# Performance work log

Hardware: AMD Instinct MI355X
Metric: run time of the kernel (lower is better)

## Reference

```python
import jax, jax.numpy as jnp
import numpy as np

B, Q, E, NH, L, P = 8, 1024, 256, 8, 4, 4
DH = E // NH
SHAPES = np.array([[128, 128], [64, 64], [32, 32], [16, 16]], dtype=np.int64)
STARTS = np.concatenate([[0], np.cumsum(SHAPES.prod(1))[:-1]]).astype(np.int64)
S_TOTAL = int(SHAPES.prod(1).sum())
EPS = 1e-5


def setup_inputs() -> dict:
    key = jax.random.key(0)
    ks = iter(jax.random.split(key, 40))
    def rn(shp, s=0.02):
        return jax.random.normal(next(ks), shp, jnp.float32) * s
    return {
        "tgt": rn((B, Q, E), 1.0),
        "query_pos": rn((B, Q, E), 1.0),
        "reference_points": jax.random.uniform(next(ks), (B, Q, L, 2), jnp.float32),
        "src": rn((B, S_TOTAL, E), 1.0),
        "spatial_shapes": jnp.asarray(SHAPES),
        "level_start_index": jnp.asarray(STARTS),
        "in_proj_w": rn((3 * E, E)), "in_proj_b": jnp.zeros((3 * E,), jnp.float32),
        "out_proj_w": rn((E, E)), "out_proj_b": jnp.zeros((E,), jnp.float32),
        "norm1_g": jnp.ones((E,), jnp.float32), "norm1_b": jnp.zeros((E,), jnp.float32),
        "off_w": rn((NH * L * P * 2, E)), "off_b": rn((NH * L * P * 2,), 0.5),
        "aw_w": rn((NH * L * P, E)), "aw_b": jnp.zeros((NH * L * P,), jnp.float32),
        "vp_w": rn((E, E)), "vp_b": jnp.zeros((E,), jnp.float32),
        "op_w": rn((E, E)), "op_b": jnp.zeros((E,), jnp.float32),
        "norm2_g": jnp.ones((E,), jnp.float32), "norm2_b": jnp.zeros((E,), jnp.float32),
        "w1": rn((4 * E, E)), "b1": jnp.zeros((4 * E,), jnp.float32),
        "w2": rn((E, 4 * E)), "b2": jnp.zeros((E,), jnp.float32),
        "norm3_g": jnp.ones((E,), jnp.float32), "norm3_b": jnp.zeros((E,), jnp.float32),
    }


def _ln(x, g, b):
    mu = x.mean(-1, keepdims=True)
    var = ((x - mu) ** 2).mean(-1, keepdims=True)
    return (x - mu) * jax.lax.rsqrt(var + EPS) * g + b


def _bilinear(v, loc, Hl, Wl):
    # v: [B,NH,S_l,DH], loc in [0,1]: [B,NH,Q,P,2] -> [B,NH,Q,P,DH]
    # matches torch grid_sample(align_corners=False, padding='zeros')
    x = loc[..., 0] * Wl - 0.5
    y = loc[..., 1] * Hl - 0.5
    x0 = jnp.floor(x)
    y0 = jnp.floor(y)
    wx = (x - x0)[..., None]
    wy = (y - y0)[..., None]
    def g(yi, xi):
        valid = ((xi >= 0) & (xi <= Wl - 1) & (yi >= 0) & (yi <= Hl - 1)).astype(v.dtype)
        idx = (jnp.clip(yi, 0, Hl - 1) * Wl + jnp.clip(xi, 0, Wl - 1)).astype(jnp.int32)
        out = jnp.take_along_axis(v, idx.reshape(B, NH, Q * P, 1), axis=2)
        return out.reshape(B, NH, Q, P, DH) * valid[..., None]
    v00 = g(y0, x0); v01 = g(y0, x0 + 1.0)
    v10 = g(y0 + 1.0, x0); v11 = g(y0 + 1.0, x0 + 1.0)
    return (v00 * (1 - wy) * (1 - wx) + v01 * (1 - wy) * wx
            + v10 * wy * (1 - wx) + v11 * wy * wx)


def _forward(tgt, query_pos, reference_points, src,
             in_proj_w, in_proj_b, out_proj_w, out_proj_b, norm1_g, norm1_b,
             off_w, off_b, aw_w, aw_b, vp_w, vp_b, op_w, op_b,
             norm2_g, norm2_b, w1, b1, w2, b2, norm3_g, norm3_b,
             spatial_shapes, level_start_index):
    shp = np.asarray(spatial_shapes)
    starts = np.asarray(level_start_index)
    # ---- self-attention (q = k = tgt + pos, v = tgt) ----
    qk = tgt + query_pos
    wq, wk, wv = jnp.split(in_proj_w, 3, axis=0)
    bq, bk, bv = jnp.split(in_proj_b, 3, axis=0)
    q = (qk @ wq.T + bq).reshape(B, Q, NH, DH)
    k = (qk @ wk.T + bk).reshape(B, Q, NH, DH)
    v = (tgt @ wv.T + bv).reshape(B, Q, NH, DH)
    scores = jnp.einsum("bqhd,bkhd->bhqk", q, k) / jnp.sqrt(jnp.float32(DH))
    attn = jax.nn.softmax(scores, axis=-1)
    ctx = jnp.einsum("bhqk,bkhd->bqhd", attn, v).reshape(B, Q, E)
    tgt = _ln(tgt + (ctx @ out_proj_w.T + out_proj_b), norm1_g, norm1_b)
    # ---- MSDA cross-attention ----
    query = tgt + query_pos
    value = (src @ vp_w.T + vp_b).reshape(B, S_TOTAL, NH, DH).transpose(0, 2, 1, 3)  # [B,NH,S,DH]
    off = (query @ off_w.T + off_b).reshape(B, Q, NH, L, P, 2)
    aw = jax.nn.softmax((query @ aw_w.T + aw_b).reshape(B, Q, NH, L * P), -1)
    aw = aw.reshape(B, Q, NH, L, P)
    normalizer = jnp.asarray(shp[:, ::-1].copy(), jnp.float32)  # [L,2] = (W,H)
    loc = reference_points[:, :, None, :, None, :] + off / normalizer[None, None, None, :, None, :]
    loc = jnp.transpose(loc, (0, 2, 1, 3, 4, 5))  # [B,NH,Q,L,P,2]
    awt = jnp.transpose(aw, (0, 2, 1, 3, 4))      # [B,NH,Q,L,P]
    out = jnp.zeros((B, NH, Q, DH), jnp.float32)
    for l in range(L):
        Hl, Wl = int(shp[l, 0]), int(shp[l, 1])
        s0 = int(starts[l])
        vl = value[:, :, s0:s0 + Hl * Wl]
        samp = _bilinear(vl, loc[:, :, :, l], Hl, Wl)         # [B,NH,Q,P,DH]
        out = out + (samp * awt[:, :, :, l, :, None]).sum(3)
    ca = out.transpose(0, 2, 1, 3).reshape(B, Q, E) @ op_w.T + op_b
    tgt = _ln(tgt + ca, norm2_g, norm2_b)
    # ---- FFN ----
    h = jax.nn.relu(tgt @ w1.T + b1) @ w2.T + b2
    return _ln(tgt + h, norm3_g, norm3_b)


def reference(tgt, query_pos, reference_points, src, spatial_shapes, level_start_index,
              in_proj_w, in_proj_b, out_proj_w, out_proj_b, norm1_g, norm1_b,
              off_w, off_b, aw_w, aw_b, vp_w, vp_b, op_w, op_b,
              norm2_g, norm2_b, w1, b1, w2, b2, norm3_g, norm3_b):
    return _forward(tgt, query_pos, reference_points, src,
                    in_proj_w, in_proj_b, out_proj_w, out_proj_b, norm1_g, norm1_b,
                    off_w, off_b, aw_w, aw_b, vp_w, vp_b, op_w, op_b,
                    norm2_g, norm2_b, w1, b1, w2, b2, norm3_g, norm3_b,
                    spatial_shapes, level_start_index)
```

## Files before the change

### kernel.cpp

```cpp
#include <hip/hip_runtime.h>
#include <hip/hip_bf16.h>
#include <math.h>

typedef __hip_bfloat16 bf16;
typedef unsigned short ushort_t;

#define BQ 8
#define QLEN 1024
#define EMB 256
#define NHD 8
#define NLVL 4
#define NPT 4
#define DHD 32
#define STOT 21760

typedef short s8v __attribute__((ext_vector_type(8)));
typedef float f4v __attribute__((ext_vector_type(4)));

__device__ __forceinline__ float b2f(bf16 x) { return __bfloat162float(x); }

__device__ __forceinline__ float ldin(const void* p, int bf, size_t i) {
    return bf ? __bfloat162float(((const bf16*)p)[i]) : ((const float*)p)[i];
}

__device__ __forceinline__ float bfraw(unsigned u) {
    union { unsigned i; float f; } c; c.i = u << 16; return c.f;
}

__device__ __forceinline__ unsigned short f2us(float x) {
    bf16 h = __float2bfloat16(x);
    unsigned short u;
    __builtin_memcpy(&u, &h, 2);
    return u;
}

__device__ __forceinline__ void ld4(const void* p, int bf, size_t i, float* o) {
    if (bf) {
        const uint2 u = *(const uint2*)((const ushort_t*)p + i);
        o[0] = bfraw(u.x & 0xffffu); o[1] = bfraw(u.x >> 16);
        o[2] = bfraw(u.y & 0xffffu); o[3] = bfraw(u.y >> 16);
    } else {
        const float4 f = *(const float4*)((const float*)p + i);
        o[0] = f.x; o[1] = f.y; o[2] = f.z; o[3] = f.w;
    }
}

typedef const __attribute__((address_space(1))) unsigned int* gas1_u32;
typedef __attribute__((address_space(3))) unsigned int* las3_u32;
__device__ __forceinline__ void gload_lds16(const void* g, void* l) {
    __builtin_amdgcn_global_load_lds((gas1_u32)g, (las3_u32)l, 16, 0, 0);
}

__global__ void detect_dtype(const unsigned* __restrict__ n1g, int* __restrict__ flag) {
    if (threadIdx.x == 0) flag[0] = (n1g[0] == 0x3F800000u) ? 0 : 1;
}

template <int BN, int KT, int WAVES, bool ARAW, bool RELU, typename CT>
__global__ __launch_bounds__(WAVES * 64) void gemm_wlds(
        const void* __restrict__ A,
        const void* __restrict__ W, int w0,
        const void* __restrict__ bias, int b0,
        CT* __restrict__ C,
        int M, int N,
        const int* __restrict__ dflag) {
    constexpr int T = WAVES * 64;
    constexpr int GPR = KT / 8;
    constexpr int WSLOTS = BN * GPR;
    constexpr int NJ = BN / 16;
    constexpr int KC = KT / 256;
    constexpr int CW = BN < 128 ? BN : 128;
    constexpr int NCH = BN / CW;
    constexpr int JC = CW / 16;
    constexpr int ST_US = (sizeof(CT) == 2) ? (CW + 8) : 2 * (CW + 12);
    constexpr int EPI_US = WAVES * 16 * ST_US;
    constexpr int SMEM_US = (BN * KT) > EPI_US ? (BN * KT) : EPI_US;

    __shared__ __align__(16) ushort_t smem[SMEM_US];

    const int bfm = *dflag;
    const int tid = threadIdx.x;
    const int lane = tid & 63;
    const int wv = tid >> 6;
    const int l15 = lane & 15, lhi = lane >> 4;
    const int n0 = blockIdx.x * BN;
    const int mg = blockIdx.y * (16 * WAVES) + wv * 16;

#pragma unroll
    for (int i = 0; i < WSLOTS / T; ++i) {
        const int s0 = (wv << 6) + T * i;
        const int s = s0 + lane;
        const int n = s / GPR;
        const int gl = s & (GPR - 1);
        const int gg = (gl + GPR - (n & (GPR - 1))) & (GPR - 1);
        const size_t woff = (size_t)(w0 + n0 + n) * KT + gg * 8;
        if (bfm) {
            gload_lds16((const ushort_t*)W + woff, smem + (size_t)s0 * 8);
        } else {
            const float* wf = (const float*)W + woff;
            const float4 f0 = *(const float4*)wf;
            const float4 f1 = *(const float4*)(wf + 4);
            ushort_t t[8] = {f2us(f0.x), f2us(f0.y), f2us(f0.z), f2us(f0.w),
                             f2us(f1.x), f2us(f1.y), f2us(f1.z), f2us(f1.w)};
            *(uint4*)(smem + (size_t)s * 8) = *(uint4*)t;
        }
    }

    auto ldA = [&](int kc, s8v* af) {
#pragma unroll
        for (int kk = 0; kk < 8; ++kk) {
            const size_t ao = (size_t)(mg + l15) * KT + kc * 256 + kk * 32 + lhi * 8;
            if (!ARAW || bfm) {
                af[kk] = *(const s8v*)((const ushort_t*)A + ao);
            } else {
                const float* ap = (const float*)A + ao;
                const float4 f0 = *(const float4*)ap;
                const float4 f1 = *(const float4*)(ap + 4);
                ushort_t t[8] = {f2us(f0.x), f2us(f0.y), f2us(f0.z), f2us(f0.w),
                                 f2us(f1.x), f2us(f1.y), f2us(f1.z), f2us(f1.w)};
                af[kk] = *(const s8v*)t;
            }
        }
    };

    f4v acc[NJ] = {};
    s8v afA[8], afB[8];
    ldA(0, afA);
    __syncthreads();

#pragma unroll
    for (int kc = 0; kc < KC; ++kc) {
        s8v* af = (kc & 1) ? afB : afA;
        s8v* afn = (kc & 1) ? afA : afB;
        if (kc + 1 < KC) ldA(kc + 1, afn);
#pragma unroll
        for (int j = 0; j < NJ; ++j) {
            const int n = j * 16 + l15;
#pragma unroll
            for (int kk = 0; kk < 8; ++kk) {
                const int gg = kc * 32 + kk * 4 + lhi;
                const int gl = (gg + n) & (GPR - 1);
                const s8v b = *(const s8v*)(smem + (size_t)n * KT + gl * 8);
                acc[j] = __builtin_amdgcn_mfma_f32_16x16x32_bf16(af[kk], b, acc[j], 0, 0, 0);
            }
        }
    }
    __syncthreads();

    if constexpr (sizeof(CT) == 2) {
        ushort_t* eb = smem + wv * 16 * ST_US;
#pragma unroll
        for (int c = 0; c < NCH; ++c) {
#pragma unroll
            for (int jj = 0; jj < JC; ++jj) {
                const int j = c * JC + jj;
                const float bv = ldin(bias, bfm, b0 + n0 + j * 16 + l15);
#pragma unroll
                for (int p = 0; p < 4; ++p) {
                    float v = acc[j][p] + bv;
                    if (RELU) v = fmaxf(v, 0.f);
                    eb[(lhi * 4 + p) * ST_US + jj * 16 + l15] = f2us(v);
                }
            }
            asm volatile("s_waitcnt lgkmcnt(0)" ::: "memory");
            __builtin_amdgcn_sched_barrier(0);
            constexpr int GPRow = CW / 8;
            constexpr int RPP = 64 / GPRow;
#pragma unroll
            for (int pass = 0; pass < 16 / RPP; ++pass) {
                const int row = pass * RPP + lane / GPRow;
                const int g = lane % GPRow;
                const uint4 u = *(const uint4*)(eb + row * ST_US + g * 8);
                *(uint4*)((ushort_t*)C + (size_t)(mg + row) * N + n0 + c * CW + g * 8) = u;
            }
            asm volatile("s_waitcnt lgkmcnt(0)" ::: "memory");
            __builtin_amdgcn_sched_barrier(0);
        }
    } else {
        constexpr int ST_F = CW + 12;
        float* ef = (float*)(smem) + wv * 16 * ST_F;
#pragma unroll
        for (int c = 0; c < NCH; ++c) {
#pragma unroll
            for (int jj = 0; jj < JC; ++jj) {
                const int j = c * JC + jj;
                const float bv = ldin(bias, bfm, b0 + n0 + j * 16 + l15);
#pragma unroll
                for (int p = 0; p < 4; ++p) {
                    float v = acc[j][p] + bv;
                    if (RELU) v = fmaxf(v, 0.f);
                    ef[(lhi * 4 + p) * ST_F + jj * 16 + l15] = v;
                }
            }
            asm volatile("s_waitcnt lgkmcnt(0)" ::: "memory");
            __builtin_amdgcn_sched_barrier(0);
            constexpr int GPRow = CW / 4;
            constexpr int RPP = 64 / GPRow;
#pragma unroll
            for (int pass = 0; pass < 16 / RPP; ++pass) {
                const int row = pass * RPP + lane / GPRow;
                const int g = lane % GPRow;
                const float4 u = *(const float4*)(ef + row * ST_F + g * 4);
                *(float4*)((float*)C + (size_t)(mg + row) * N + n0 + c * CW + g * 4) = u;
            }
            asm volatile("s_waitcnt lgkmcnt(0)" ::: "memory");
            __builtin_amdgcn_sched_barrier(0);
        }
    }
}

__global__ void ew_add_bf(const void* __restrict__ a, const void* __restrict__ b,
                          ushort_t* __restrict__ c, int n4, const int* __restrict__ dflag) {
    const int bfm = *dflag;
    const int i = blockIdx.x * 256 + threadIdx.x;
    if (i < n4) {
        float ta[4], tb[4];
        ld4(a, bfm, (size_t)i * 4, ta);
        ld4(b, bfm, (size_t)i * 4, tb);
        uint2 u;
        u.x = (unsigned)f2us(ta[0] + tb[0]) | ((unsigned)f2us(ta[1] + tb[1]) << 16);
        u.y = (unsigned)f2us(ta[2] + tb[2]) | ((unsigned)f2us(ta[3] + tb[3]) << 16);
        *(uint2*)(c + (size_t)i * 4) = u;
    }
}

__global__ __launch_bounds__(256) void attn_mfma(const ushort_t* __restrict__ qkbuf,
                                                 const ushort_t* __restrict__ v,
                                                 ushort_t* __restrict__ ctx) {
    __shared__ ushort_t Ks[64][40];
    __shared__ ushort_t Vt[32][72];
    __shared__ ushort_t Ps[4][16][72];
    const int bh = blockIdx.y;
    const int b = bh >> 3, h = bh & 7;
    const int qt = blockIdx.x;
    const int tid = threadIdx.x;
    const int lane = tid & 63;
    const int wv = tid >> 6;
    const int l15 = lane & 15, quad = lane >> 4;
    const float scale = 0.17677669529663689f;

    const int qbase = (qt << 6) + (wv << 4);
    const s8v qfrag = *(const s8v*)(qkbuf +
        ((size_t)(b * QLEN + qbase + l15)) * 512 + h * DHD + quad * 8);

    const int sk = tid >> 2;
    const int sd = (tid & 3) << 3;

    float m_run[4] = {-1e30f, -1e30f, -1e30f, -1e30f};
    float l_run[4] = {};
    f4v o[2] = {};

    for (int kt = 0; kt < 16; ++kt) {
        __syncthreads();
        const size_t krow = (size_t)(b * QLEN + (kt << 6) + sk);
        *(uint4*)&Ks[sk][sd] = *(const uint4*)(qkbuf + krow * 512 + 256 + h * DHD + sd);
        const uint4 uv = *(const uint4*)(v + krow * 256 + h * DHD + sd);
        ushort_t vt[8];
        *(uint4*)vt = uv;
#pragma unroll
        for (int j = 0; j < 8; ++j) Vt[sd + j][sk] = vt[j];
        __syncthreads();

        f4v s4[4];
#pragma unroll
        for (int kb = 0; kb < 4; ++kb) {
            const s8v kfr = *(const s8v*)&Ks[(kb << 4) + l15][quad * 8];
            s4[kb] = __builtin_amdgcn_mfma_f32_16x16x32_bf16(qfrag, kfr, f4v{}, 0, 0, 0);
        }

        float sc[4][4];
#pragma unroll
        for (int kb = 0; kb < 4; ++kb)
#pragma unroll
            for (int p = 0; p < 4; ++p) sc[kb][p] = s4[kb][p] * scale;
        float mp[4];
#pragma unroll
        for (int p = 0; p < 4; ++p)
            mp[p] = fmaxf(fmaxf(sc[0][p], sc[1][p]), fmaxf(sc[2][p], sc[3][p]));
#pragma unroll
        for (int p = 0; p < 4; ++p) {
            mp[p] = fmaxf(mp[p], __shfl_xor(mp[p], 1, 64));
            mp[p] = fmaxf(mp[p], __shfl_xor(mp[p], 2, 64));
            mp[p] = fmaxf(mp[p], __shfl_xor(mp[p], 4, 64));
            mp[p] = fmaxf(mp[p], __shfl_xor(mp[p], 8, 64));
        }
        float al[4], ls[4] = {};
#pragma unroll
        for (int p = 0; p < 4; ++p) {
            const float mn = fmaxf(m_run[p], mp[p]);
            al[p] = __expf(m_run[p] - mn);
            m_run[p] = mn;
        }
        float pe[4][4];
#pragma unroll
        for (int kb = 0; kb < 4; ++kb)
#pragma unroll
            for (int p = 0; p < 4; ++p) {
                const float e = __expf(sc[kb][p] - m_run[p]);
                pe[kb][p] = e;
                ls[p] += e;
            }
#pragma unroll
        for (int p = 0; p < 4; ++p) {
            ls[p] += __shfl_xor(ls[p], 1, 64);
            ls[p] += __shfl_xor(ls[p], 2, 64);
            ls[p] += __shfl_xor(ls[p], 4, 64);
            ls[p] += __shfl_xor(ls[p], 8, 64);
            l_run[p] = l_run[p] * al[p] + ls[p];
        }
#pragma unroll
        for (int nb = 0; nb < 2; ++nb)
#pragma unroll
            for (int p = 0; p < 4; ++p) o[nb][p] *= al[p];

#pragma unroll
        for (int kb = 0; kb < 4; ++kb)
#pragma unroll
            for (int p = 0; p < 4; ++p)
                Ps[wv][(quad << 2) + p][(kb << 4) + l15] = f2us(pe[kb][p]);

#pragma unroll
        for (int kk = 0; kk < 2; ++kk) {
            const s8v afr = *(const s8v*)&Ps[wv][l15][kk * 32 + quad * 8];
#pragma unroll
            for (int nb = 0; nb < 2; ++nb) {
                const s8v bfr = *(const s8v*)&Vt[nb * 16 + l15][kk * 32 + quad * 8];
                o[nb] = __builtin_amdgcn_mfma_f32_16x16x32_bf16(afr, bfr, o[nb], 0, 0, 0);
            }
        }
    }

#pragma unroll
    for (int p = 0; p < 4; ++p) {
        const float inv = 1.f / l_run[p];
        const size_t row = (size_t)(b * QLEN + qbase + (quad << 2) + p) * EMB + h * DHD;
#pragma unroll
        for (int nb = 0; nb < 2; ++nb)
            ctx[row + nb * 16 + l15] = f2us(o[nb][p] * inv);
    }
}

__global__ __launch_bounds__(256) void ln_kernel(const void* __restrict__ xb,
                                                 const float* __restrict__ xf1,
                                                 const float* __restrict__ xf2,
                                                 const void* __restrict__ g,
                                                 const void* __restrict__ bta,
                                                 float* __restrict__ out_f,
                                                 ushort_t* __restrict__ out_b,
                                                 void* __restrict__ out_d,
                                                 const void* __restrict__ qp,
                                                 ushort_t* __restrict__ out_q,
                                                 const int* __restrict__ dflag) {
    const int bf = *dflag;
    const int row = blockIdx.x * 4 + (threadIdx.x >> 6);
    const int lane = threadIdx.x & 63;
    const size_t base = (size_t)row * EMB + lane * 4;

    float x[4] = {0.f, 0.f, 0.f, 0.f};
    if (xb) {
        float t[4]; ld4(xb, bf, base, t);
#pragma unroll
        for (int j = 0; j < 4; ++j) x[j] += t[j];
    }
    if (xf1) {
        const float4 f = *(const float4*)(xf1 + base);
        x[0] += f.x; x[1] += f.y; x[2] += f.z; x[3] += f.w;
    }
    if (xf2) {
        const float4 f = *(const float4*)(xf2 + base);
        x[0] += f.x; x[1] += f.y; x[2] += f.z; x[3] += f.w;
    }
    float s = x[0] + x[1] + x[2] + x[3];
#pragma unroll
    for (int o = 1; o < 64; o <<= 1) s += __shfl_xor(s, o, 64);
    const float mu = s * (1.f / EMB);
    float dx[4], vs = 0.f;
#pragma unroll
    for (int j = 0; j < 4; ++j) { dx[j] = x[j] - mu; vs += dx[j] * dx[j]; }
#pragma unroll
    for (int o = 1; o < 64; o <<= 1) vs += __shfl_xor(vs, o, 64);
    const float inv = rsqrtf(vs * (1.f / EMB) + 1e-5f);

    float gv[4], bv[4];
    ld4(g, bf, (size_t)lane * 4, gv);
    ld4(bta, bf, (size_t)lane * 4, bv);
    float y[4];
#pragma unroll
    for (int j = 0; j < 4; ++j) y[j] = dx[j] * inv * gv[j] + bv[j];

    if (out_f) *(float4*)(out_f + base) = float4{y[0], y[1], y[2], y[3]};
    if (out_b) {
        uint2 u;
        u.x = (unsigned)f2us(y[0]) | ((unsigned)f2us(y[1]) << 16);
        u.y = (unsigned)f2us(y[2]) | ((unsigned)f2us(y[3]) << 16);
        *(uint2*)(out_b + base) = u;
    }
    if (out_d) {
        if (bf) {
            uint2 u;
            u.x = (unsigned)f2us(y[0]) | ((unsigned)f2us(y[1]) << 16);
            u.y = (unsigned)f2us(y[2]) | ((unsigned)f2us(y[3]) << 16);
            *(uint2*)((ushort_t*)out_d + base) = u;
        } else {
            *(float4*)((float*)out_d + base) = float4{y[0], y[1], y[2], y[3]};
        }
    }
    if (out_q) {
        float q[4]; ld4(qp, bf, base, q);
        uint2 u;
        u.x = (unsigned)f2us(y[0] + q[0]) | ((unsigned)f2us(y[1] + q[1]) << 16);
        u.y = (unsigned)f2us(y[2] + q[2]) | ((unsigned)f2us(y[3] + q[3]) << 16);
        *(uint2*)(out_q + base) = u;
    }
}

__global__ __launch_bounds__(64) void sample_kernel(const float* __restrict__ offb,
                                                    const float* __restrict__ awb,
                                                    const void* __restrict__ refp,
                                                    const ushort_t* __restrict__ value,
                                                    ushort_t* __restrict__ out,
                                                    const int* __restrict__ dflag) {
    const int bf = *dflag;
    const int bid = blockIdx.x;
    const int h = bid & 7;
    const int bq = bid >> 3;
    const int b = bq >> 10;
    const int lane = threadIdx.x;
    const int s_idx = lane >> 2;
    const int dg = lane & 3;
    const int l = s_idx >> 2;

    float logit = awb[(size_t)bq * 128 + h * 16 + s_idx];
    float m = logit;
#pragma unroll
    for (int o = 32; o > 0; o >>= 1) m = fmaxf(m, __shfl_xor(m, o, 64));
    float e = __expf(logit - m);
    float ssum = e;
#pragma unroll
    for (int o = 32; o > 0; o >>= 1) ssum += __shfl_xor(ssum, o, 64);
    const float paw = 4.f * e / ssum;

    const int Wi = 128 >> l;
    const float Wl = (float)Wi, Hl = (float)Wi;
    const int s0 = (l == 0) ? 0 : (l == 1) ? 16384 : (l == 2) ? 20480 : 21504;

    const float rx = ldin(refp, bf, ((size_t)bq * NLVL + l) * 2 + 0);
    const float ry = ldin(refp, bf, ((size_t)bq * NLVL + l) * 2 + 1);
    const float ox = offb[(size_t)bq * 256 + h * 32 + s_idx * 2 + 0];
    const float oy = offb[(size_t)bq * 256 + h * 32 + s_idx * 2 + 1];
    const float x = (rx + ox / Wl) * Wl - 0.5f;
    const float y = (ry + oy / Hl) * Hl - 0.5f;
    const float x0 = floorf(x), y0 = floorf(y);
    const float wx = x - x0, wy = y - y0;

    float acc[8] = {};
    const ushort_t* vbase = value + ((size_t)b * STOT) * EMB + h * DHD + dg * 8;

    auto corner = [&](float yi, float xi, float w) {
        const bool valid = (xi >= 0.f) && (xi <= Wl - 1.f) && (yi >= 0.f) && (yi <= Hl - 1.f);
        const float xc = fminf(fmaxf(xi, 0.f), Wl - 1.f);
        const float yc = fminf(fmaxf(yi, 0.f), Hl - 1.f);
        const int row = s0 + (int)yc * Wi + (int)xc;
        const uint4 u = *(const uint4*)(vbase + (size_t)row * EMB);
        const float wv = valid ? w : 0.f;
        const unsigned ua[4] = {u.x, u.y, u.z, u.w};
#pragma unroll
        for (int j = 0; j < 4; ++j) {
            acc[2 * j + 0] = fmaf(wv, bfraw(ua[j] & 0xffffu), acc[2 * j + 0]);
            acc[2 * j + 1] = fmaf(wv, bfraw(ua[j] >> 16), acc[2 * j + 1]);
        }
    };
    corner(y0, x0, (1.f - wy) * (1.f - wx));
    corner(y0, x0 + 1.f, (1.f - wy) * wx);
    corner(y0 + 1.f, x0, wy * (1.f - wx));
    corner(y0 + 1.f, x0 + 1.f, wy * wx);

#pragma unroll
    for (int j = 0; j < 8; ++j) {
        float vj = acc[j] * paw;
        vj += __shfl_xor(vj, 4, 64);
        vj += __shfl_xor(vj, 8, 64);
        vj += __shfl_xor(vj, 16, 64);
        vj += __shfl_xor(vj, 32, 64);
        acc[j] = vj;
    }
    if (s_idx == 0) {
        ushort_t t[8];
#pragma unroll
        for (int j = 0; j < 8; ++j) t[j] = f2us(acc[j]);
        *(uint4*)(out + (size_t)bq * EMB + h * DHD + dg * 8) = *(uint4*)t;
    }
}

extern "C" void kernel_launch(void* const* d_in, const int* in_sizes, int n_in,
                              void* d_out, int out_size, void* d_ws, size_t ws_size,
                              hipStream_t stream) {
    const void* tgt  = d_in[0];
    const void* qp   = d_in[1];
    const void* refp = d_in[2];
    const void* src  = d_in[3];
    const void* ipw  = d_in[6];
    const void* ipb  = d_in[7];
    const void* oprw = d_in[8];
    const void* oprb = d_in[9];
    const void* n1g  = d_in[10];
    const void* n1b  = d_in[11];
    const void* ofw  = d_in[12];
    const void* ofb  = d_in[13];
    const void* aww  = d_in[14];
    const void* awbv = d_in[15];
    const void* vpw  = d_in[16];
    const void* vpb  = d_in[17];
    const void* opw2 = d_in[18];
    const void* opb2 = d_in[19];
    const void* n2g  = d_in[20];
    const void* n2b  = d_in[21];
    const void* w1   = d_in[22];
    const void* b1   = d_in[23];
    const void* w2   = d_in[24];
    const void* b2   = d_in[25];
    const void* n3g  = d_in[26];
    const void* n3b  = d_in[27];

    const int M = BQ * QLEN;
    const int MS = BQ * STOT;

    char* ws = (char*)d_ws;
    int* dflag = (int*)ws;
    size_t o = 256;
    char* S1 = ws + o; o += (size_t)M * EMB * 2;
    char* S2 = ws + o; o += (size_t)M * 512 * 2;
    char* S3 = ws + o; o += (size_t)M * EMB * 2;
    char* S4 = ws + o; o += (size_t)M * EMB * 2;
    char* S5 = ws + o; o += (size_t)M * EMB * 4;
    char* S6 = ws + o; o += (size_t)M * EMB * 4;
    char* S7 = ws + o; o += (size_t)M * EMB * 4;
    char* S8 = ws + o;

    ushort_t* qk_bf    = (ushort_t*)S1;
    ushort_t* samp_bf  = (ushort_t*)S1;
    ushort_t* qkproj   = (ushort_t*)S2;
    float*    off_f    = (float*)S2;
    ushort_t* vproj    = (ushort_t*)S3;
    ushort_t* qry_bf   = (ushort_t*)S3;
    ushort_t* tgt2_bf  = (ushort_t*)S3;
    ushort_t* ctx_bf   = (ushort_t*)S4;
    float*    awl_f    = (float*)S4;
    float*    bufD     = (float*)S5;
    float*    tgt1_f   = (float*)S6;
    float*    tgt2_f   = (float*)S7;
    ushort_t* value_bf = (ushort_t*)S8;
    ushort_t* h1_bf    = (ushort_t*)S8;

    detect_dtype<<<1, 64, 0, stream>>>((const unsigned*)n1g, dflag);

    ew_add_bf<<<(M * EMB / 4) / 256, 256, 0, stream>>>(tgt, qp, qk_bf, M * EMB / 4, dflag);
    gemm_wlds<64, 256, 4, false, false, ushort_t><<<dim3(8, M / 64), 256, 0, stream>>>(
        qk_bf, ipw, 0, ipb, 0, qkproj, M, 512, dflag);
    gemm_wlds<64, 256, 4, true, false, ushort_t><<<dim3(4, M / 64), 256, 0, stream>>>(
        tgt, ipw, 512, ipb, 512, vproj, M, 256, dflag);
    attn_mfma<<<dim3(16, BQ * NHD), 256, 0, stream>>>(qkproj, vproj, ctx_bf);
    gemm_wlds<64, 256, 4, false, false, float><<<dim3(4, M / 64), 256, 0, stream>>>(
        ctx_bf, oprw, 0, oprb, 0, bufD, M, 256, dflag);
    ln_kernel<<<M / 4, 256, 0, stream>>>(tgt, bufD, nullptr, n1g, n1b,
                                         tgt1_f, nullptr, nullptr, qp, qry_bf, dflag);

    gemm_wlds<64, 256, 4, false, false, float><<<dim3(4, M / 64), 256, 0, stream>>>(
        qry_bf, ofw, 0, ofb, 0, off_f, M, 256, dflag);
    gemm_wlds<64, 256, 4, false, false, float><<<dim3(2, M / 64), 256, 0, stream>>>(
        qry_bf, aww, 0, awbv, 0, awl_f, M, 128, dflag);
    gemm_wlds<256, 256, 16, true, false, ushort_t><<<dim3(1, MS / 256), 1024, 0, stream>>>(
        src, vpw, 0, vpb, 0, value_bf, MS, 256, dflag);
    sample_kernel<<<M * NHD, 64, 0, stream>>>(off_f, awl_f, refp, value_bf, samp_bf, dflag);
    gemm_wlds<64, 256, 4, false, false, float><<<dim3(4, M / 64), 256, 0, stream>>>(
        samp_bf, opw2, 0, opb2, 0, bufD, M, 256, dflag);
    ln_kernel<<<M / 4, 256, 0, stream>>>(nullptr, tgt1_f, bufD, n2g, n2b,
                                         tgt2_f, tgt2_bf, nullptr, nullptr, nullptr, dflag);

    gemm_wlds<64, 256, 4, false, true, ushort_t><<<dim3(16, M / 64), 256, 0, stream>>>(
        tgt2_bf, w1, 0, b1, 0, h1_bf, M, 1024, dflag);
    gemm_wlds<32, 1024, 4, false, false, float><<<dim3(8, M / 64), 256, 0, stream>>>(
        h1_bf, w2, 0, b2, 0, bufD, M, 256, dflag);
    ln_kernel<<<M / 4, 256, 0, stream>>>(nullptr, tgt2_f, bufD, n3g, n3b,
                                         nullptr, nullptr, d_out, nullptr, nullptr, dflag);
}
```

Measured before the change: 596.5 us.

## Stage activation tile in LDS and hold weight fragments in registers per wave

The GEMM kernel is restructured so the shared A (activation) tile of BM rows is staged in LDS with an XOR swizzle. Each wave now loads its own 32-column slice of the weight matrix into registers and iterates over row groups, where before each wave owned 16 rows and the whole weight tile sat in LDS. All launches move to 64x128 (or 32x128) tiles, and the large value projection drops from 1024-thread blocks to 256-thread blocks. The aim is to reuse weights across more rows and cut LDS footprint to raise occupancy. The cost is more register pressure from holding weights per wave and a barrier per K chunk.

```diff
diff --git a/kernel.cpp b/kernel.cpp
--- a/kernel.cpp
+++ b/kernel.cpp
@@ -55,8 +55,8 @@
     if (threadIdx.x == 0) flag[0] = (n1g[0] == 0x3F800000u) ? 0 : 1;
 }
 
-template <int BN, int KT, int WAVES, bool ARAW, bool RELU, typename CT>
-__global__ __launch_bounds__(WAVES * 64) void gemm_wlds(
+template <int BM, int BN, int WAVES, int KT, bool ARAW, bool RELU, typename CT>
+__global__ __launch_bounds__(WAVES * 64) void gemm_alds(
         const void* __restrict__ A,
         const void* __restrict__ W, int w0,
         const void* __restrict__ bias, int b0,
@@ -64,143 +64,133 @@
         int M, int N,
         const int* __restrict__ dflag) {
     constexpr int T = WAVES * 64;
-    constexpr int GPR = KT / 8;
-    constexpr int WSLOTS = BN * GPR;
-    constexpr int NJ = BN / 16;
+    constexpr int NT = BN / (16 * WAVES);
+    constexpr int RG = BM / 16;
     constexpr int KC = KT / 256;
-    constexpr int CW = BN < 128 ? BN : 128;
-    constexpr int NCH = BN / CW;
-    constexpr int JC = CW / 16;
-    constexpr int ST_US = (sizeof(CT) == 2) ? (CW + 8) : 2 * (CW + 12);
-    constexpr int EPI_US = WAVES * 16 * ST_US;
-    constexpr int SMEM_US = (BN * KT) > EPI_US ? (BN * KT) : EPI_US;
-
-    __shared__ __align__(16) ushort_t smem[SMEM_US];
+    constexpr int ASLOTS = BM * 32;
+
+    __shared__ __align__(16) ushort_t smem[BM * 256];
 
     const int bfm = *dflag;
     const int tid = threadIdx.x;
     const int lane = tid & 63;
     const int wv = tid >> 6;
     const int l15 = lane & 15, lhi = lane >> 4;
+    const int swz = l15 & 7;
     const int n0 = blockIdx.x * BN;
-    const int mg = blockIdx.y * (16 * WAVES) + wv * 16;
-
-#pragma unroll
-    for (int i = 0; i < WSLOTS / T; ++i) {
-        const int s0 = (wv << 6) + T * i;
-        const int s = s0 + lane;
-        const int n = s / GPR;
-        const int gl = s & (GPR - 1);
-        const int gg = (gl + GPR - (n & (GPR - 1))) & (GPR - 1);
-        const size_t woff = (size_t)(w0 + n0 + n) * KT + gg * 8;
-        if (bfm) {
-            gload_lds16((const ushort_t*)W + woff, smem + (size_t)s0 * 8);
-        } else {
-            const float* wf = (const float*)W + woff;
-            const float4 f0 = *(const float4*)wf;
-            const float4 f1 = *(const float4*)(wf + 4);
-            ushort_t t[8] = {f2us(f0.x), f2us(f0.y), f2us(f0.z), f2us(f0.w),
-                             f2us(f1.x), f2us(f1.y), f2us(f1.z), f2us(f1.w)};
-            *(uint4*)(smem + (size_t)s * 8) = *(uint4*)t;
-        }
-    }
-
-    auto ldA = [&](int kc, s8v* af) {
-#pragma unroll
-        for (int kk = 0; kk < 8; ++kk) {
-            const size_t ao = (size_t)(mg + l15) * KT + kc * 256 + kk * 32 + lhi * 8;
+    const int bm0 = blockIdx.y * BM;
+    const int cb = n0 + wv * (NT * 16);
+
+    auto stageA = [&](int kc) {
+#pragma unroll
+        for (int i = 0; i < ASLOTS / T; ++i) {
+            const int s0 = (wv << 6) + T * i;
+            const int s = s0 + lane;
+            const int r = s >> 5;
+            const int gl = s & 31;
+            const int gg = gl ^ (r & 7);
+            const size_t aoff = (size_t)(bm0 + r) * KT + kc * 256 + gg * 8;
             if (!ARAW || bfm) {
-                af[kk] = *(const s8v*)((const ushort_t*)A + ao);
+                gload_lds16((const ushort_t*)A + aoff, smem + (size_t)s0 * 8);
             } else {
-                const float* ap = (const float*)A + ao;
+                const float* ap = (const float*)A + aoff;
                 const float4 f0 = *(const float4*)ap;
                 const float4 f1 = *(const float4*)(ap + 4);
                 ushort_t t[8] = {f2us(f0.x), f2us(f0.y), f2us(f0.z), f2us(f0.w),
                                  f2us(f1.x), f2us(f1.y), f2us(f1.z), f2us(f1.w)};
-                af[kk] = *(const s8v*)t;
+                *(uint4*)(smem + (size_t)s * 8) = *(uint4*)t;
             }
         }
     };
 
-    f4v acc[NJ] = {};
-    s8v afA[8], afB[8];
-    ldA(0, afA);
+    s8v bw[NT][8];
+    auto loadW = [&](int kc) {
+#pragma unroll
+        for (int j = 0; j < NT; ++j)
+#pragma unroll
+            for (int kk = 0; kk < 8; ++kk) {
+                const size_t woff = (size_t)(w0 + cb + j * 16 + l15) * KT
+                                  + kc * 256 + kk * 32 + lhi * 8;
+                if (bfm) {
+                    bw[j][kk] = *(const s8v*)((const ushort_t*)W + woff);
+                } else {
+                    const float* wp = (const float*)W + woff;
+                    const float4 f0 = *(const float4*)wp;
+                    const float4 f1 = *(const float4*)(wp + 4);
+                    ushort_t t[8] = {f2us(f0.x), f2us(f0.y), f2us(f0.z), f2us(f0.w),
+                                     f2us(f1.x), f2us(f1.y), f2us(f1.z), f2us(f1.w)};
+                    bw[j][kk] = *(const s8v*)t;
+                }
+            }
+    };
+
+    f4v acc[RG][NT] = {};
+
+#pragma unroll
+    for (int kc = 0; kc < KC; ++kc) {
+        stageA(kc);
+        loadW(kc);
+        __syncthreads();
+#pragma unroll
+        for (int rg = 0; rg < RG; ++rg) {
+#pragma unroll
+            for (int kk = 0; kk < 8; ++kk) {
+                const int gl = (kk * 4 + lhi) ^ swz;
+                const s8v a = *(const s8v*)(smem + (size_t)(rg * 16 + l15) * 256 + gl * 8);
+#pragma unroll
+                for (int j = 0; j < NT; ++j)
+                    acc[rg][j] = __builtin_amdgcn_mfma_f32_16x16x32_bf16(
+                        a, bw[j][kk], acc[rg][j], 0, 0, 0);
+            }
+        }
+        if (kc + 1 < KC) __syncthreads();
+    }
     __syncthreads();
 
-#pragma unroll
-    for (int kc = 0; kc < KC; ++kc) {
-        s8v* af = (kc & 1) ? afB : afA;
-        s8v* afn = (kc & 1) ? afA : afB;
-        if (kc + 1 < KC) ldA(kc + 1, afn);
-#pragma unroll
-        for (int j = 0; j < NJ; ++j) {
-            const int n = j * 16 + l15;
-#pragma unroll
-            for (int kk = 0; kk < 8; ++kk) {
-                const int gg = kc * 32 + kk * 4 + lhi;
-                const int gl = (gg + n) & (GPR - 1);
-                const s8v b = *(const s8v*)(smem + (size_t)n * KT + gl * 8);
-                acc[j] = __builtin_amdgcn_mfma_f32_16x16x32_bf16(af[kk], b, acc[j], 0, 0, 0);
-            }
-        }
-    }
-    __syncthreads();
-
     if constexpr (sizeof(CT) == 2) {
-        ushort_t* eb = smem + wv * 16 * ST_US;
-#pragma unroll
-        for (int c = 0; c < NCH; ++c) {
-#pragma unroll
-            for (int jj = 0; jj < JC; ++jj) {
-                const int j = c * JC + jj;
-                const float bv = ldin(bias, bfm, b0 + n0 + j * 16 + l15);
+        ushort_t* eb = smem + wv * 16 * 40;
+#pragma unroll
+        for (int rg = 0; rg < RG; ++rg) {
+#pragma unroll
+            for (int j = 0; j < NT; ++j) {
+                const float bv = ldin(bias, bfm, b0 + cb + j * 16 + l15);
 #pragma unroll
                 for (int p = 0; p < 4; ++p) {
-                    float v = acc[j][p] + bv;
+                    float v = acc[rg][j][p] + bv;
                     if (RELU) v = fmaxf(v, 0.f);
-                    eb[(lhi * 4 + p) * ST_US + jj * 16 + l15] = f2us(v);
+                    eb[(lhi * 4 + p) * 40 + j * 16 + l15] = f2us(v);
                 }
             }
             asm volatile("s_waitcnt lgkmcnt(0)" ::: "memory");
             __builtin_amdgcn_sched_barrier(0);
-            constexpr int GPRow = CW / 8;
-            constexpr int RPP = 64 / GPRow;
-#pragma unroll
-            for (int pass = 0; pass < 16 / RPP; ++pass) {
-                const int row = pass * RPP + lane / GPRow;
-                const int g = lane % GPRow;
-                const uint4 u = *(const uint4*)(eb + row * ST_US + g * 8);
-                *(uint4*)((ushort_t*)C + (size_t)(mg + row) * N + n0 + c * CW + g * 8) = u;
-            }
+            const int row = lane >> 2, g = lane & 3;
+            const uint4 u = *(const uint4*)(eb + row * 40 + g * 8);
+            *(uint4*)((ushort_t*)C + (size_t)(bm0 + rg * 16 + row) * N + cb + g * 8) = u;
             asm volatile("s_waitcnt lgkmcnt(0)" ::: "memory");
             __builtin_amdgcn_sched_barrier(0);
         }
     } else {
-        constexpr int ST_F = CW + 12;
-        float* ef = (float*)(smem) + wv * 16 * ST_F;
-#pragma unroll
-        for (int c = 0; c < NCH; ++c) {
-#pragma unroll
-            for (int jj = 0; jj < JC; ++jj) {
-                const int j = c * JC + jj;
-                const float bv = ldin(bias, bfm, b0 + n0 + j * 16 + l15);
+        float* ef = (float*)smem + wv * 16 * 36;
+#pragma unroll
+        for (int rg = 0; rg < RG; ++rg) {
+#pragma unroll
+            for (int j = 0; j < NT; ++j) {
+                const float bv = ldin(bias, bfm, b0 + cb + j * 16 + l15);
 #pragma unroll
                 for (int p = 0; p < 4; ++p) {
-                    float v = acc[j][p] + bv;
+                    float v = acc[rg][j][p] + bv;
                     if (RELU) v = fmaxf(v, 0.f);
-                    ef[(lhi * 4 + p) * ST_F + jj * 16 + l15] = v;
+                    ef[(lhi * 4 + p) * 36 + j * 16 + l15] = v;
                 }
             }
             asm volatile("s_waitcnt lgkmcnt(0)" ::: "memory");
             __builtin_amdgcn_sched_barrier(0);
-            constexpr int GPRow = CW / 4;
-            constexpr int RPP = 64 / GPRow;
-#pragma unroll
-            for (int pass = 0; pass < 16 / RPP; ++pass) {
-                const int row = pass * RPP + lane / GPRow;
-                const int g = lane % GPRow;
-                const float4 u = *(const float4*)(ef + row * ST_F + g * 4);
-                *(float4*)((float*)C + (size_t)(mg + row) * N + n0 + c * CW + g * 4) = u;
+#pragma unroll
+            for (int pass = 0; pass < 2; ++pass) {
+                const int row = pass * 8 + (lane >> 3);
+                const int g = lane & 7;
+                const float4 u = *(const float4*)(ef + row * 36 + g * 4);
+                *(float4*)((float*)C + (size_t)(bm0 + rg * 16 + row) * N + cb + g * 4) = u;
             }
             asm volatile("s_waitcnt lgkmcnt(0)" ::: "memory");
             __builtin_amdgcn_sched_barrier(0);
@@ -554,31 +544,31 @@
     detect_dtype<<<1, 64, 0, stream>>>((const unsigned*)n1g, dflag);
 
     ew_add_bf<<<(M * EMB / 4) / 256, 256, 0, stream>>>(tgt, qp, qk_bf, M * EMB / 4, dflag);
-    gemm_wlds<64, 256, 4, false, false, ushort_t><<<dim3(8, M / 64), 256, 0, stream>>>(
+    gemm_alds<64, 128, 4, 256, false, false, ushort_t><<<dim3(4, M / 64), 256, 0, stream>>>(
         qk_bf, ipw, 0, ipb, 0, qkproj, M, 512, dflag);
-    gemm_wlds<64, 256, 4, true, false, ushort_t><<<dim3(4, M / 64), 256, 0, stream>>>(
+    gemm_alds<64, 128, 4, 256, true, false, ushort_t><<<dim3(2, M / 64), 256, 0, stream>>>(
         tgt, ipw, 512, ipb, 512, vproj, M, 256, dflag);
     attn_mfma<<<dim3(16, BQ * NHD), 256, 0, stream>>>(qkproj, vproj, ctx_bf);
-    gemm_wlds<64, 256, 4, false, false, float><<<dim3(4, M / 64), 256, 0, stream>>>(
+    gemm_alds<64, 128, 4, 256, false, false, float><<<dim3(2, M / 64), 256, 0, stream>>>(
         ctx_bf, oprw, 0, oprb, 0, bufD, M, 256, dflag);
     ln_kernel<<<M / 4, 256, 0, stream>>>(tgt, bufD, nullptr, n1g, n1b,
                                          tgt1_f, nullptr, nullptr, qp, qry_bf, dflag);
 
-    gemm_wlds<64, 256, 4, false, false, float><<<dim3(4, M / 64), 256, 0, stream>>>(
+    gemm_alds<64, 128, 4, 256, false, false, float><<<dim3(2, M / 64), 256, 0, stream>>>(
         qry_bf, ofw, 0, ofb, 0, off_f, M, 256, dflag);
-    gemm_wlds<64, 256, 4, false, false, float><<<dim3(2, M / 64), 256, 0, stream>>>(
+    gemm_alds<32, 128, 4, 256, false, false, float><<<dim3(1, M / 32), 256, 0, stream>>>(
         qry_bf, aww, 0, awbv, 0, awl_f, M, 128, dflag);
-    gemm_wlds<256, 256, 16, true, false, ushort_t><<<dim3(1, MS / 256), 1024, 0, stream>>>(
+    gemm_alds<64, 128, 4, 256, true, false, ushort_t><<<dim3(2, MS / 64), 256, 0, stream>>>(
         src, vpw, 0, vpb, 0, value_bf, MS, 256, dflag);
     sample_kernel<<<M * NHD, 64, 0, stream>>>(off_f, awl_f, refp, value_bf, samp_bf, dflag);
-    gemm_wlds<64, 256, 4, false, false, float><<<dim3(4, M / 64), 256, 0, stream>>>(
+    gemm_alds<64, 128, 4, 256, false, false, float><<<dim3(2, M / 64), 256, 0, stream>>>(
         samp_bf, opw2, 0, opb2, 0, bufD, M, 256, dflag);
     ln_kernel<<<M / 4, 256, 0, stream>>>(nullptr, tgt1_f, bufD, n2g, n2b,
                                          tgt2_f, tgt2_bf, nullptr, nullptr, nullptr, dflag);
 
-    gemm_wlds<64, 256, 4, false, true, ushort_t><<<dim3(16, M / 64), 256, 0, stream>>>(
+    gemm_alds<64, 128, 4, 256, false, true, ushort_t><<<dim3(8, M / 64), 256, 0, stream>>>(
         tgt2_bf, w1, 0, b1, 0, h1_bf, M, 1024, dflag);
-    gemm_wlds<32, 1024, 4, false, false, float><<<dim3(8, M / 64), 256, 0, stream>>>(
+    gemm_alds<64, 128, 4, 1024, false, false, float><<<dim3(2, M / 64), 256, 0, stream>>>(
         h1_bf, w2, 0, b2, 0, bufD, M, 256, dflag);
     ln_kernel<<<M / 4, 256, 0, stream>>>(nullptr, tgt2_f, bufD, n3g, n3b,
                                          nullptr, nullptr, d_out, nullptr, nullptr, dflag);
```

New measurement: 685.2 us. 1.15x slower.
